# Optimization experiments

Hardware: AMD Instinct MI355X
Metric: run time of the kernel (lower is better)

## Reference

```python
import jax, jax.numpy as jnp
import numpy as np

N = 20000      # nodes (drugs, scaled to production size)
E = 640000     # edges
R = 65         # relation types
F_IN = 128     # input feature dim (trimnet embedding)
H1 = 64        # hidden1
H2 = 32        # hidden2 (bilinear discriminator dim)
B = 8192       # drug pairs in idx


def setup_inputs() -> dict:
    key = jax.random.key(0)
    ks = jax.random.split(key, 20)
    s = 0.05
    return {
        "x_o": jax.random.normal(ks[0], (N, F_IN), jnp.float32),
        "x_a": jax.random.normal(ks[1], (N, F_IN), jnp.float32),
        "features1": jax.random.normal(ks[2], (N, F_IN), jnp.float32),
        "W1": jax.random.normal(ks[3], (R, F_IN, H1), jnp.float32) * s,
        "root1": jax.random.normal(ks[4], (F_IN, H1), jnp.float32) * s,
        "b1": jnp.zeros((H1,), jnp.float32),
        "W2": jax.random.normal(ks[5], (R, H1, H2), jnp.float32) * s,
        "root2": jax.random.normal(ks[6], (H1, H2), jnp.float32) * s,
        "b2": jnp.zeros((H2,), jnp.float32),
        "attt": jnp.array([0.5, 0.5], jnp.float32),
        "disc_W": jax.random.normal(ks[7], (H2, H2), jnp.float32) * s,
        "disc_b": jnp.zeros((), jnp.float32),
        "cls_W": jax.random.normal(ks[8], (448, R), jnp.float32) * s,
        "cls_b": jnp.zeros((R,), jnp.float32),
        "edge_index": jax.random.randint(ks[9], (2, E), 0, N, jnp.int32),
        "e_type": jax.random.randint(ks[10], (E,), 0, R, jnp.int32),
        "e_type1": jax.random.randint(ks[11], (E,), 0, R, jnp.int32),
        "idx": jax.random.randint(ks[12], (2, B), 0, N, jnp.int32),
    }


def rgcn(x, src, dst, etype, W, root, b):
    """RGCNConv with per-relation mean aggregation (PyG default aggr='mean').
    Aggregates source features per (relation, dst) via one segment_sum, then
    applies the relation weights once with a batched matmul."""
    n, fin = x.shape
    seg = etype * n + dst                       # combined (relation, dst) segment id
    msg = x[src]                                # [E, fin] gather
    agg = jax.ops.segment_sum(msg, seg, num_segments=R * n).reshape(R, n, fin)
    cnt = jax.ops.segment_sum(jnp.ones((src.shape[0],), x.dtype), seg,
                              num_segments=R * n).reshape(R, n, 1)
    agg = agg / jnp.maximum(cnt, 1.0)           # per-relation mean
    out = jnp.einsum('rnf,rfh->nh', agg, W)     # sum over relations of W_r @ mean_r
    return out + x @ root + b


def reference(x_o, x_a, features1, W1, root1, b1, W2, root2, b2, attt,
              disc_W, disc_b, cls_W, cls_b, edge_index, e_type, e_type1, idx):
    src, dst = edge_index[0], edge_index[1]

    def enc(x, et):
        h1 = jax.nn.relu(rgcn(x, src, dst, et, W1, root1, b1))
        # dropout is identity in eval mode
        h2 = rgcn(h1, src, dst, et, W2, root2, b2)
        return h1, h2

    x1_o, x2_o = enc(x_o, e_type)
    _, x2_o_a = enc(x_a, e_type)
    _, x2_o_a_a = enc(x_o, e_type1)

    c = jax.nn.sigmoid(jnp.mean(x2_o, axis=0))  # readout + sigmoid, [H2]

    def disc(h_pl, h_mi):
        s1 = h_pl @ disc_W @ c + disc_b         # bilinear f_k(h, c)
        s2 = h_mi @ disc_W @ c + disc_b
        return jnp.stack([s1, s2], axis=1)      # [N, 2]

    ret_os = disc(x2_o, x2_o_a)
    ret_os_a = disc(x2_o, x2_o_a_a)

    final = jnp.concatenate([attt[0] * x1_o, attt[1] * x2_o], axis=1)  # [N, 96]
    e1 = jnp.concatenate([final[idx[0]], features1[idx[0]]], axis=1)   # [B, 224]
    e2 = jnp.concatenate([final[idx[1]], features1[idx[1]]], axis=1)
    log = jnp.concatenate([e1, e2], axis=1) @ cls_W + cls_b            # [B, 65]
    return (log, ret_os, ret_os_a, x2_o)
```

## Files before the change

kernel.cpp:

```cpp
#include <hip/hip_runtime.h>
#include <hip/hip_bf16.h>

#define NN 20000
#define EE 640000
#define RR 65
#define FIN1 128
#define HH1 64
#define HH2 32
#define BB 8192

constexpr int BM = 128;
constexpr int GBM = 256;
constexpr int NBH = 256;
constexpr int GRID_PRE = 2048;
constexpr int EPB = EE / NBH;
constexpr int NBT = (NN + BM - 1) / BM;
constexpr int NOCT = 8;
constexpr int NPO = NN / NOCT;
constexpr int NB2 = NOCT * RR;
constexpr int MAXT2 = EE / GBM + NB2;

constexpr int CLS_K  = 512;
constexpr int CLS_N  = 80;
constexpr int CLS_CK = 128;
constexpr int CLS_BM = 64;

typedef __attribute__((ext_vector_type(8))) short short8;
typedef __attribute__((ext_vector_type(4))) float floatx4;
typedef __attribute__((ext_vector_type(4))) unsigned int uint4e;
typedef __attribute__((ext_vector_type(2))) unsigned int uint2e;

constexpr size_t aln(size_t x) { return (x + 255) & ~(size_t)255; }

constexpr size_t OFF_CSUM  = 0;
constexpr size_t OFF_CNTD  = aln(OFF_CSUM + 32 * 4);
constexpr size_t ZERO_BYTES = OFF_CNTD + (size_t)NN * 4;
constexpr size_t OFF_DSTOFF = aln(ZERO_BYTES);
constexpr size_t OFF_BH0   = aln(OFF_DSTOFF + ((size_t)NN + 1) * 4);
constexpr size_t OFF_BH1   = OFF_BH0 + (size_t)NBH * NB2 * 4;
constexpr size_t OFF_BB0   = OFF_BH1 + (size_t)NBH * NB2 * 4;
constexpr size_t OFF_BB1   = OFF_BB0 + (size_t)NBH * NB2 * 4;
constexpr size_t OFF_HT    = aln(OFF_BB1 + (size_t)NBH * NB2 * 4);
constexpr size_t OFF_OFFB0 = aln(OFF_HT + (size_t)2 * NB2 * 4);
constexpr size_t OFF_OFFB1 = OFF_OFFB0 + (NB2 + 1) * 4;
constexpr size_t OFF_TILB0 = aln(OFF_OFFB1 + (NB2 + 1) * 4);
constexpr size_t OFF_TILT0 = OFF_TILB0 + (size_t)MAXT2 * 4;
constexpr size_t OFF_TILB1 = OFF_TILT0 + (size_t)MAXT2 * 4;
constexpr size_t OFF_TILT1 = OFF_TILB1 + (size_t)MAXT2 * 4;
// ... 21 lines not shown
constexpr size_t MSG_B2    = (size_t)EE * HH2 * 2;
constexpr size_t WS_END    = OFF_MSG + MSG_B1;

constexpr size_t O_LOG  = 0;
constexpr size_t O_ROS  = (size_t)BB * RR;
constexpr size_t O_ROSA = O_ROS + (size_t)NN * 2;
constexpr size_t O_X2O  = O_ROSA + (size_t)NN * 2;

__device__ inline unsigned short f2bf(float f) {
    __hip_bfloat16 h = __float2bfloat16(f);
    return *reinterpret_cast<unsigned short*>(&h);
}
__device__ inline float bfbits2f(unsigned int hi_bits) {
    return __uint_as_float(hi_bits);
}

struct GemmEnc {
    const unsigned short* X;
    unsigned short* msg;
    const unsigned int* perm;
    const int* offB;
    const int* tilB;
    const int* tilT;
};
struct GemmArgs { GemmEnc e[3]; };

struct RedEnc {
    const unsigned short* msg;
    const float* wD;
    float* base;
    unsigned short* bfout;
};
struct RedArgs { RedEnc e[3]; };

__global__ void k_hist(const int* __restrict__ ei, const int* __restrict__ et0,
                       const int* __restrict__ et1,
                       int* cntD, int* __restrict__ slotE,
                       int* __restrict__ bh0, int* __restrict__ bh1,
                       const float* __restrict__ x_o, const float* __restrict__ x_a,
                       const float* __restrict__ W1, const float* __restrict__ W2,
                       const float* __restrict__ root1, const float* __restrict__ root2,
                       const float* __restrict__ clsW,
                       unsigned short* xob, unsigned short* xab,
                       unsigned short* w1t, unsigned short* w2t,
                       unsigned short* r1t, unsigned short* r2t,
                       unsigned short* cwt) {
// ... 65 lines not shown
    for (int i4 = i0; i4 < NR2_4; i4 += stride) {
        int i = i4 * 4;
        int k = i % HH1; int hh = i / HH1;
        const float* s = &root2[(size_t)k * HH2 + hh];
        uint2 pk;
        pk.x = (unsigned)f2bf(s[0]) | ((unsigned)f2bf(s[HH2]) << 16);
        pk.y = (unsigned)f2bf(s[2 * HH2]) | ((unsigned)f2bf(s[3 * HH2]) << 16);
        ((uint2*)r2t)[i4] = pk;
    }
    const int NCW_4 = CLS_N * CLS_K / 4;
    for (int i4 = i0; i4 < NCW_4; i4 += stride) {
        int i = i4 * 4;
        int k = i % CLS_K; int n = i / CLS_K;
        uint2 pk = {0u, 0u};
        if (n < RR && k < 448) {
            const float* s = &clsW[(size_t)k * RR + n];
            pk.x = (unsigned)f2bf(s[0]) | ((unsigned)f2bf(s[RR]) << 16);
            pk.y = (unsigned)f2bf(s[2 * RR]) | ((unsigned)f2bf(s[3 * RR]) << 16);
        }
        ((uint2*)cwt)[i4] = pk;
    }
}

__global__ void k_scanD(const int* __restrict__ cntD, int* __restrict__ dstOff) {
    __shared__ int s[256];
    int t = threadIdx.x;
    constexpr int PER = (NN + 255) / 256;
    int lo = t * PER, hi = min(NN, lo + PER);
    int sum = 0;
    for (int i = lo; i < hi; i++) sum += cntD[i];
    s[t] = sum;
    __syncthreads();
    for (int ofs = 1; ofs < 256; ofs <<= 1) {
        int v = 0;
        if (t >= ofs) v = s[t - ofs];
        __syncthreads();
        if (t >= ofs) s[t] += v;
        __syncthreads();
    }
    int run = s[t] - sum;
    for (int i = lo; i < hi; i++) { dstOff[i] = run; run += cntD[i]; }
    if (t == 255) dstOff[NN] = run;
}

__global__ void k_post(const int* __restrict__ ei, const int* __restrict__ et0,
                       const int* __restrict__ et1, const int* __restrict__ dstOff,
                       const int* __restrict__ slotE,
                       int* __restrict__ posD, unsigned int* __restrict__ rdP) {
    int e = blockIdx.x * 256 + threadIdx.x;
    if (e < EE) {
        int d = ei[EE + e];
        int pos = dstOff[d] + slotE[e];
        posD[e] = pos;
        rdP[pos] = (unsigned)et0[e] | ((unsigned)et1[e] << 16);
    }
}

__global__ void k_scanB1(const int* __restrict__ bh0, const int* __restrict__ bh1,
                         int* __restrict__ bb0, int* __restrict__ bb1,
                         int* __restrict__ hT) {
    int w = (blockIdx.x * 256 + threadIdx.x) >> 6;
    int lane = threadIdx.x & 63;
    if (w >= 2 * NB2) return;
    int s = w / NB2, k = w % NB2;
    const int* bh = s ? bh1 : bh0;
    int* bb = s ? bb1 : bb0;
    int v[4];
    #pragma unroll
    for (int i = 0; i < 4; i++) v[i] = bh[(size_t)(lane * 4 + i) * NB2 + k];
    int ls = v[0] + v[1] + v[2] + v[3];
    int inc = ls;
    #pragma unroll
    for (int ofs = 1; ofs < 64; ofs <<= 1) {
        int o = __shfl_up(inc, ofs);
        if (lane >= ofs) inc += o;
    }
    int run = inc - ls;
    #pragma unroll
    for (int i = 0; i < 4; i++) {
        bb[(size_t)(lane * 4 + i) * NB2 + k] = run;
        run += v[i];
    }
    if (lane == 63) hT[s * NB2 + k] = run;
}

__global__ void k_scanB2(const int* __restrict__ hT,
                         int* offB0, int* offB1,
                         int* tilB0, int* tilT0, int* tilB1, int* tilT1) {
    __shared__ int h[2][NB2];
    __shared__ int o[2][NB2 + 1];
    __shared__ int to[2][NB2 + 1];
    __shared__ int csumE[2][8], csumT[2][8];
    int t = threadIdx.x;
    for (int p = t; p < 2 * NB2; p += 256) h[p / NB2][p % NB2] = hT[p];
    __syncthreads();
    if (t < 16) {
        int s = t / 8, c = t % 8;
        int runE = 0, runT = 0;
        for (int k = c * RR; k < (c + 1) * RR; k++) {
            o[s][k] = runE;  runE += h[s][k];
            to[s][k] = runT; runT += (h[s][k] + GBM - 1) / GBM;
        }
        csumE[s][c] = runE; csumT[s][c] = runT;
    }
    __syncthreads();
    if (t < 2) {
        int runE = 0, runT = 0;
        for (int c = 0; c < 8; c++) {
            int e = csumE[t][c], tt = csumT[t][c];
            csumE[t][c] = runE; csumT[t][c] = runT;
            runE += e; runT += tt;
        }
        o[t][NB2] = runE; to[t][NB2] = runT;
    }
    __syncthreads();
    if (t < 16) {
// ... 2 lines not shown
            o[s][k] += csumE[s][c];
            to[s][k] += csumT[s][c];
        }
    }
    __syncthreads();
    for (int p = t; p <= NB2; p += 256) { offB0[p] = o[0][p]; offB1[p] = o[1][p]; }
    for (int i = t; i < MAXT2; i += 256) {
        #pragma unroll
        for (int s = 0; s < 2; s++) {
            int total = to[s][NB2];
            int bkt = -1, ti = 0;
            if (i < total) {
                int lo = 0, hi = NB2;
                while (hi - lo > 1) { int mid = (lo + hi) >> 1; if (to[s][mid] <= i) lo = mid; else hi = mid; }
                bkt = lo;
                ti = i - to[s][lo];
            }
            if (s == 0) { tilB0[i] = bkt; tilT0[i] = ti; }
            else        { tilB1[i] = bkt; tilT1[i] = ti; }
        }
    }
}

__global__ void k_fillB(const int* __restrict__ ei, const int* __restrict__ et0,
                        const int* __restrict__ et1, const int* __restrict__ posD,
                        const int* __restrict__ offB0, const int* __restrict__ offB1,
                        const int* __restrict__ bb0, const int* __restrict__ bb1,
                        unsigned int* perm0, unsigned int* perm1) {
    __shared__ int lc[2][NB2];
    __shared__ int lb[2][NB2];
    int t = threadIdx.x;
    for (int p = t; p < NB2; p += 256) {
        lc[0][p] = 0; lc[1][p] = 0;
        lb[0][p] = offB0[p] + bb0[blockIdx.x * NB2 + p];
        lb[1][p] = offB1[p] + bb1[blockIdx.x * NB2 + p];
    }
    __syncthreads();
    int base = blockIdx.x * EPB;
    for (int i = t; i < EPB; i += 256) {
        int e = base + i;
        int src = ei[e];
        int pos = posD[e];
        int oct = src / NPO;
        unsigned int packed = ((unsigned)(src - oct * NPO) << 20) | (unsigned)pos;
        int k0 = oct * RR + et0[e];
        int k1 = oct * RR + et1[e];
        int p0 = atomicAdd(&lc[0][k0], 1);
        int p1 = atomicAdd(&lc[1][k1], 1);
        perm0[lb[0][k0] + p0] = packed;
        perm1[lb[1][k1] + p1] = packed;
    }
}

__global__ void k_wts(const int* __restrict__ dstOff, const unsigned int* __restrict__ rdP,
                      float* __restrict__ wD0, float* __restrict__ wD1) {
    constexpr int CAP = 96;
    __shared__ unsigned int ld[4][CAP];
    int wave = threadIdx.x >> 6;
    int lane = threadIdx.x & 63;
    int d = blockIdx.x * 4 + wave;
    int j0 = 0, deg = 0;
    if (d < NN) { j0 = dstOff[d]; deg = dstOff[d + 1] - j0; }
    for (int j = lane; j < deg && j < CAP; j += 64) ld[wave][j] = rdP[j0 + j];
    __syncthreads();
    for (int j = lane; j < deg; j += 64) {
        unsigned int my = (j < CAP) ? ld[wave][j] : rdP[j0 + j];
        unsigned int m0 = my & 0xffffu, m1 = my >> 16;
        int c0 = 0, c1 = 0;
        for (int k = 0; k < deg; k++) {
            unsigned int p = (k < CAP) ? ld[wave][k] : rdP[j0 + k];
            c0 += ((p & 0xffffu) == m0);
            c1 += ((p >> 16) == m1);
        }
        wD0[j0 + j] = 1.0f / (float)c0;
        wD1[j0 + j] = 1.0f / (float)c1;
    }
}

template <int FIN, int HOUT>
__launch_bounds__(256, 3)
__global__ void k_bgemm(const unsigned short* __restrict__ X0,
                        const unsigned short* __restrict__ X1,
                        const unsigned short* __restrict__ X2,
// ... 46 lines not shown
    for (int ks = 0; ks < KS; ks++) {
        int kk = ks * 32 + q * 8;
        short8 af0 = *(const short8*)&As[mbase + ln][kk];
        short8 af1 = *(const short8*)&As[mbase + 16 + ln][kk];
        #pragma unroll
        for (int nt = 0; nt < NT; nt++) {
            short8 bf = *(const short8*)&Bs[nt * 16 + ln][kk];
            acc[0][nt] = __builtin_amdgcn_mfma_f32_16x16x32_bf16(af0, bf, acc[0][nt], 0, 0, 0);
            acc[1][nt] = __builtin_amdgcn_mfma_f32_16x16x32_bf16(af1, bf, acc[1][nt], 0, 0, 0);
        }
    }

    #pragma unroll
    for (int mt = 0; mt < 2; mt++) {
        #pragma unroll
        for (int rr2 = 0; rr2 < 4; rr2++) {
            int i = mbase + mt * 16 + q * 4 + rr2;
            int n = n0 + i;
            if (i < mcount) {
                #pragma unroll
                for (int nt = 0; nt < NT; nt++)
                    O[(size_t)n * HOUT + nt * 16 + ln] = acc[mt][nt][rr2] + bias[nt * 16 + ln];
            }
        }
    }
}

template <int FIN, int HOUT>
__launch_bounds__(512, 8)
__global__ void k_gemm(GemmArgs ga, const unsigned short* __restrict__ WT) {
    const GemmEnc ge = ga.e[blockIdx.y];
    int b = blockIdx.x;
    int bkt = ge.tilB[b];
    if (bkt < 0) return;
    int r = bkt % RR;
    int srcBase = (bkt / RR) * NPO;
    int t = ge.tilT[b];
    int ebase = ge.offB[bkt] + t * GBM;
    int mcount = min(GBM, ge.offB[bkt + 1] - ebase);

    constexpr int LDK = FIN + 8;
    constexpr int LDM = HOUT + 8;
    constexpr int BSZ = HOUT * LDK;
    constexpr int MSZ = GBM * LDM;
    constexpr int USZ = BSZ > MSZ ? BSZ : MSZ;
    __shared__ unsigned short Us[USZ];
// ... 120 lines not shown
        re.base[o] = v0; re.base[o + 1] = v1; re.base[o + 2] = v2; re.base[o + 3] = v3;
        if (RELU) {
            re.bfout[o] = f2bf(v0); re.bfout[o + 1] = f2bf(v1);
            re.bfout[o + 2] = f2bf(v2); re.bfout[o + 3] = f2bf(v3);
        }
    }
}

__global__ void k_mean(const float* __restrict__ x2o, float* __restrict__ part) {
    __shared__ float s[256];
    int t = threadIdx.x; int hh = t & 31; int g = t >> 5;
    float acc = 0.f;
    for (int n = blockIdx.x * 8 + g; n < NN; n += gridDim.x * 8)
        acc += x2o[(size_t)n * 32 + hh];
    s[t] = acc;
    __syncthreads();
    if (t < 32) {
        float v = 0.f;
        for (int gg = 0; gg < 8; gg++) v += s[gg * 32 + t];
        part[blockIdx.x * 32 + t] = v;
    }
}

__global__ void k_csum(const float* __restrict__ part, float* __restrict__ csum) {
    int t = threadIdx.x;
    if (t < 32) {
        double a = 0.0;
        for (int b = 0; b < 256; b++) a += (double)part[b * 32 + t];
        csum[t] = (float)a;
    }
}

__global__ void k_disc(const float* __restrict__ x2o, const float* __restrict__ x2a,
                       const float* __restrict__ x2aa, const float* __restrict__ csum,
                       const float* __restrict__ discW, const float* __restrict__ discb,
                       float* ret_os, float* ret_osa) {
    __shared__ float c[32], v[32];
    int t = threadIdx.x;
    if (t < 32) c[t] = 1.f / (1.f + expf(-csum[t] * (1.f / NN)));
    __syncthreads();
    if (t < 32) {
        float a = 0.f;
        for (int j = 0; j < 32; j++) a += discW[t * 32 + j] * c[j];
        v[t] = a;
    }
    __syncthreads();
    float db = discb[0];
    int n = blockIdx.x * 256 + t;
    if (n < NN) {
        float s1 = 0.f, s2 = 0.f, s3 = 0.f;
        for (int j = 0; j < 32; j++) {
            float vj = v[j];
            s1 += x2o[(size_t)n * 32 + j] * vj;
            s2 += x2a[(size_t)n * 32 + j] * vj;
            s3 += x2aa[(size_t)n * 32 + j] * vj;
        }
        ret_os[n * 2] = s1 + db;  ret_os[n * 2 + 1] = s2 + db;
        ret_osa[n * 2] = s1 + db; ret_osa[n * 2 + 1] = s3 + db;
    }
}

__launch_bounds__(256, 2)
__global__ void k_clsg(const float* __restrict__ h1o, const float* __restrict__ x2o,
                       const float* __restrict__ feat, const float* __restrict__ attt,
                       const int* __restrict__ idx,
                       const unsigned short* __restrict__ cwt,
                       const float* __restrict__ clsb, float* __restrict__ log_out) {
    constexpr int LDK = CLS_CK + 8;
    __shared__ unsigned short As[CLS_BM][LDK];
    __shared__ unsigned short Bs[CLS_N][LDK];
    __shared__ int nd[2][CLS_BM];

    int tid = threadIdx.x;
    int p0 = blockIdx.x * CLS_BM;
    if (tid < CLS_BM) {
        nd[0][tid] = idx[p0 + tid];
        nd[1][tid] = idx[BB + p0 + tid];
    }
    float a0 = attt[0], a1 = attt[1];

    const int wave = tid >> 6;
    const int lane = tid & 63;
    const int q = lane >> 4;
    const int ln = lane & 15;
    constexpr int NT = CLS_N / 16;
    const int mbase = wave * 16;

    floatx4 acc[NT];
    #pragma unroll
    for (int nt = 0; nt < NT; nt++) acc[nt] = floatx4{0.f, 0.f, 0.f, 0.f};

    for (int ch = 0; ch < CLS_K / CLS_CK; ch++) {
        int kbase = ch * CLS_CK;
        __syncthreads();
        for (int c = tid; c < CLS_N * CLS_CK / 8; c += 256) {
            int row = c / (CLS_CK / 8), cc = c % (CLS_CK / 8);
            *(uint4*)&Bs[row][cc * 8] = *(const uint4*)&cwt[(size_t)row * CLS_K + kbase + cc * 8];
        }
        for (int c = tid; c < CLS_BM * CLS_CK / 4; c += 256) {
            int row = c / (CLS_CK / 4);
            int j4 = (c % (CLS_CK / 4)) * 4;
            int j = kbase + j4;
            float4 v = {0.f, 0.f, 0.f, 0.f};
            if (j < 448) {
                int hseg = j / 224, jj = j % 224;
                int node = nd[hseg][row];
                if (jj < 64) {
                    v = *(const float4*)&h1o[(size_t)node * 64 + jj];
                    v.x *= a0; v.y *= a0; v.z *= a0; v.w *= a0;
                } else if (jj < 96) {
                    v = *(const float4*)&x2o[(size_t)node * 32 + (jj - 64)];
                    v.x *= a1; v.y *= a1; v.z *= a1; v.w *= a1;
                } else {
                    v = *(const float4*)&feat[(size_t)node * 128 + (jj - 96)];
                }
            }
            uint2 pk;
            pk.x = (unsigned)f2bf(v.x) | ((unsigned)f2bf(v.y) << 16);
            pk.y = (unsigned)f2bf(v.z) | ((unsigned)f2bf(v.w) << 16);
            *(uint2*)&As[row][j4] = pk;
        }
        __syncthreads();
        #pragma unroll
        for (int ks = 0; ks < CLS_CK / 32; ks++) {
            int kk = ks * 32 + q * 8;
            short8 af = *(const short8*)&As[mbase + ln][kk];
            #pragma unroll
            for (int nt = 0; nt < NT; nt++) {
                short8 bf = *(const short8*)&Bs[nt * 16 + ln][kk];
                acc[nt] = __builtin_amdgcn_mfma_f32_16x16x32_bf16(af, bf, acc[nt], 0, 0, 0);
            }
        }
    }

    #pragma unroll
    for (int rr2 = 0; rr2 < 4; rr2++) {
        int i = mbase + q * 4 + rr2;
        int pair = p0 + i;
        #pragma unroll
        for (int nt = 0; nt < NT; nt++) {
            int col = nt * 16 + ln;
            if (col < RR)
                log_out[(size_t)pair * RR + col] = acc[nt][rr2] + clsb[col];
        }
    }
}

extern "C" void kernel_launch(void* const* d_in, const int* in_sizes, int n_in,
                              void* d_out, int out_size, void* d_ws, size_t ws_size,
                              hipStream_t stream) {
    const float* x_o   = (const float*)d_in[0];
    const float* x_a   = (const float*)d_in[1];
    const float* feat  = (const float*)d_in[2];
    const float* W1    = (const float*)d_in[3];
    const float* root1 = (const float*)d_in[4];
    const float* b1    = (const float*)d_in[5];
    const float* W2    = (const float*)d_in[6];
    const float* root2 = (const float*)d_in[7];
    const float* b2    = (const float*)d_in[8];
    const float* attt  = (const float*)d_in[9];
    const float* discW = (const float*)d_in[10];
    const float* discb = (const float*)d_in[11];
    const float* clsW  = (const float*)d_in[12];
    const float* clsb  = (const float*)d_in[13];
    const int* ei      = (const int*)d_in[14];
    const int* et0     = (const int*)d_in[15];
    const int* et1     = (const int*)d_in[16];
    const int* idx     = (const int*)d_in[17];

    char* ws = (char*)d_ws;
    float* csum = (float*)(ws + OFF_CSUM);
    int* cntD  = (int*)(ws + OFF_CNTD);
    int* dstOff = (int*)(ws + OFF_DSTOFF);
    int* bh0   = (int*)(ws + OFF_BH0);
    int* bh1   = (int*)(ws + OFF_BH1);
    int* bb0   = (int*)(ws + OFF_BB0);
    int* bb1   = (int*)(ws + OFF_BB1);
    int* hT    = (int*)(ws + OFF_HT);
    int* offB0 = (int*)(ws + OFF_OFFB0);
    int* offB1 = (int*)(ws + OFF_OFFB1);
    int* tilB0 = (int*)(ws + OFF_TILB0);
    int* tilT0 = (int*)(ws + OFF_TILT0);
    int* tilB1 = (int*)(ws + OFF_TILB1);
    int* tilT1 = (int*)(ws + OFF_TILT1);
    int* slotE = (int*)(ws + OFF_SLOT);
    int* posD  = (int*)(ws + OFF_POSD);
    unsigned int* rdP = (unsigned int*)(ws + OFF_RDP);
    float* wD0 = (float*)(ws + OFF_WD0);
    float* wD1 = (float*)(ws + OFF_WD1);
    unsigned int* perm0 = (unsigned int*)(ws + OFF_PERM0);
    unsigned int* perm1 = (unsigned int*)(ws + OFF_PERM1);
    unsigned short* xob = (unsigned short*)(ws + OFF_XOB);
    unsigned short* xab = (unsigned short*)(ws + OFF_XAB);
    float* h1o  = (float*)(ws + OFF_H1);
    float* h1a  = h1o + (size_t)NN * HH1;
    float* h1aa = h1a + (size_t)NN * HH1;
    unsigned short* h1bo  = (unsigned short*)(ws + OFF_H1B);
    unsigned short* h1ba  = h1bo + (size_t)NN * HH1;
    unsigned short* h1baa = h1ba + (size_t)NN * HH1;
    float* x2a  = (float*)(ws + OFF_X2A);
    float* x2aa = (float*)(ws + OFF_X2AA);
    unsigned short* w1t = (unsigned short*)(ws + OFF_W1BT);
    unsigned short* w2t = (unsigned short*)(ws + OFF_W2BT);
    unsigned short* r1t = (unsigned short*)(ws + OFF_R1T);
    unsigned short* r2t = (unsigned short*)(ws + OFF_R2T);
    unsigned short* cwt = (unsigned short*)(ws + OFF_CWT);
    float* part = (float*)(ws + OFF_PART);
    unsigned short* msg = (unsigned short*)(ws + OFF_MSG);

    float* out = (float*)d_out;
    float* log_out = out + O_LOG;
    float* ret_os  = out + O_ROS;
    float* ret_osa = out + O_ROSA;
    float* x2o     = out + O_X2O;

    size_t availMsg = ws_size > OFF_MSG ? ws_size - OFF_MSG : MSG_B1;
    int nb1 = (availMsg >= 2 * MSG_B1) ? 2 : 1;
    int nb2 = (availMsg >= 3 * MSG_B2) ? 3 : (availMsg >= 2 * MSG_B2 ? 2 : 1);

    hipMemsetAsync(ws, 0, ZERO_BYTES, stream);

    k_hist<<<GRID_PRE, 256, 0, stream>>>(ei, et0, et1, cntD, slotE, bh0, bh1,
                                         x_o, x_a, W1, W2, root1, root2, clsW,
                                         xob, xab, w1t, w2t, r1t, r2t, cwt);
    k_scanD<<<1, 256, 0, stream>>>(cntD, dstOff);
    k_post<<<2500, 256, 0, stream>>>(ei, et0, et1, dstOff, slotE, posD, rdP);
    k_scanB1<<<(2 * NB2 + 3) / 4, 256, 0, stream>>>(bh0, bh1, bb0, bb1, hT);
    k_scanB2<<<1, 256, 0, stream>>>(hT, offB0, offB1,
                                    tilB0, tilT0, tilB1, tilT1);
    k_fillB<<<NBH, 256, 0, stream>>>(ei, et0, et1, posD, offB0, offB1, bb0, bb1,
                                     perm0, perm1);
    k_wts<<<NN / 4, 256, 0, stream>>>(dstOff, rdP, wD0, wD1);

    {
        dim3 gb(NBT, 3);
        k_bgemm<FIN1, HH1><<<gb, 256, 0, stream>>>(xob, xab, xob, r1t, b1,
                                                   h1o, h1a, h1aa);
        const unsigned short* Xs[3] = {xob, xab, xob};
        float* Os[3] = {h1o, h1a, h1aa};
        unsigned short* Obs[3] = {h1bo, h1ba, h1baa};
        for (int e0 = 0; e0 < 3; ) {
            int g = 3 - e0 < nb1 ? 3 - e0 : nb1;
            GemmArgs ga{};
            RedArgs ra{};
            for (int j = 0; j < g; j++) {
                int enc = e0 + j;
                unsigned short* mb = msg + (size_t)j * EE * HH1;
                ga.e[j].X    = Xs[enc];
                ga.e[j].msg  = mb;
                ga.e[j].perm = enc == 2 ? perm1 : perm0;
                ga.e[j].offB = enc == 2 ? offB1 : offB0;
                ga.e[j].tilB = enc == 2 ? tilB1 : tilB0;
                ga.e[j].tilT = enc == 2 ? tilT1 : tilT0;
                ra.e[j].msg  = mb;
                ra.e[j].wD   = enc == 2 ? wD1 : wD0;
                ra.e[j].base = Os[enc];
                ra.e[j].bfout = Obs[enc];
            }
            k_gemm<FIN1, HH1><<<dim3(MAXT2, g), 512, 0, stream>>>(ga, w1t);
            k_reduce<HH1, true><<<dim3(NN / 4, g), 256, 0, stream>>>(ra, dstOff);
            e0 += g;
        }
    }

    {
        dim3 gb(NBT, 3);
        k_bgemm<HH1, HH2><<<gb, 256, 0, stream>>>(h1bo, h1ba, h1baa, r2t, b2,
                                                  x2o, x2a, x2aa);
        const unsigned short* Xs[3] = {h1bo, h1ba, h1baa};
        float* Os[3] = {x2o, x2a, x2aa};
        for (int e0 = 0; e0 < 3; ) {
            int g = 3 - e0 < nb2 ? 3 - e0 : nb2;
            GemmArgs ga{};
            RedArgs ra{};
            for (int j = 0; j < g; j++) {
                int enc = e0 + j;
                unsigned short* mb = msg + (size_t)j * EE * HH2;
                ga.e[j].X    = Xs[enc];
                ga.e[j].msg  = mb;
                ga.e[j].perm = enc == 2 ? perm1 : perm0;
                ga.e[j].offB = enc == 2 ? offB1 : offB0;
                ga.e[j].tilB = enc == 2 ? tilB1 : tilB0;
                ga.e[j].tilT = enc == 2 ? tilT1 : tilT0;
                ra.e[j].msg  = mb;
                ra.e[j].wD   = enc == 2 ? wD1 : wD0;
                ra.e[j].base = Os[enc];
                ra.e[j].bfout = nullptr;
            }
            k_gemm<HH1, HH2><<<dim3(MAXT2, g), 512, 0, stream>>>(ga, w2t);
            k_reduce<HH2, false><<<dim3(NN / 4, g), 256, 0, stream>>>(ra, dstOff);
            e0 += g;
        }
    }

    k_mean<<<256, 256, 0, stream>>>(x2o, part);
    k_csum<<<1, 64, 0, stream>>>(part, csum);
    k_disc<<<(NN + 255) / 256, 256, 0, stream>>>(x2o, x2a, x2aa, csum, discW, discb,
                                                 ret_os, ret_osa);
    k_clsg<<<BB / CLS_BM, 256, 0, stream>>>(h1o, x2o, feat, attt, idx, cwt, clsb, log_out);
}
```

Before: 555.8 us.

## Merge preprocessing, root-GEMM, and tail kernels into fewer block-partitioned launches

Independent kernels are merged into single launches that pick their role by block index: the dst scan with the bucket scan, the post pass with the tile-table build, the bucket fill with the degree-weight pass, and the classifier GEMM with the discriminator (which now folds in the readout sum). The root/bias GEMM is folded into the per-relation message GEMM launch, and layer 1 now processes all three encoders in one launch when workspace allows. The aim is to cut kernel launch count and the idle gaps between small dependent kernels. In exchange, each fused kernel carries the union of shared memory and register needs, which may lower occupancy, and layer 1 needs a larger message buffer.

```diff
diff --git a/kernel.cpp b/kernel.cpp
--- a/kernel.cpp
+++ b/kernel.cpp
@@ -24,6 +24,8 @@
 constexpr int CLS_N  = 80;
 constexpr int CLS_CK = 128;
 constexpr int CLS_BM = 64;
+constexpr int NCLSB  = BB / CLS_BM;
+constexpr int NDISCB = (NN + 255) / 256;
 
 typedef __attribute__((ext_vector_type(8))) short short8;
 typedef __attribute__((ext_vector_type(4))) float floatx4;
@@ -91,6 +93,7 @@
     const int* offB;
     const int* tilB;
     const int* tilT;
+    float* obase;
 };
 struct GemmArgs { GemmEnc e[3]; };
 
@@ -202,45 +205,33 @@
     }
 }
 
-__global__ void k_scanD(const int* __restrict__ cntD, int* __restrict__ dstOff) {
-    __shared__ int s[256];
+__global__ void k_scanA(const int* __restrict__ cntD, int* __restrict__ dstOff,
+                        const int* __restrict__ bh0, const int* __restrict__ bh1,
+                        int* __restrict__ bb0, int* __restrict__ bb1,
+                        int* __restrict__ hT) {
     int t = threadIdx.x;
-    constexpr int PER = (NN + 255) / 256;
-    int lo = t * PER, hi = min(NN, lo + PER);
-    int sum = 0;
-    for (int i = lo; i < hi; i++) sum += cntD[i];
-    s[t] = sum;
-    __syncthreads();
-    for (int ofs = 1; ofs < 256; ofs <<= 1) {
-        int v = 0;
-        if (t >= ofs) v = s[t - ofs];
+    if (blockIdx.x == 0) {
+        __shared__ int s[256];
+        constexpr int PER = (NN + 255) / 256;
+        int lo = t * PER, hi = min(NN, lo + PER);
+        int sum = 0;
+        for (int i = lo; i < hi; i++) sum += cntD[i];
+        s[t] = sum;
         __syncthreads();
-        if (t >= ofs) s[t] += v;
-        __syncthreads();
-    }
-    int run = s[t] - sum;
-    for (int i = lo; i < hi; i++) { dstOff[i] = run; run += cntD[i]; }
-    if (t == 255) dstOff[NN] = run;
-}
-
-__global__ void k_post(const int* __restrict__ ei, const int* __restrict__ et0,
-                       const int* __restrict__ et1, const int* __restrict__ dstOff,
-                       const int* __restrict__ slotE,
-                       int* __restrict__ posD, unsigned int* __restrict__ rdP) {
-    int e = blockIdx.x * 256 + threadIdx.x;
-    if (e < EE) {
-        int d = ei[EE + e];
-        int pos = dstOff[d] + slotE[e];
-        posD[e] = pos;
-        rdP[pos] = (unsigned)et0[e] | ((unsigned)et1[e] << 16);
-    }
-}
-
-__global__ void k_scanB1(const int* __restrict__ bh0, const int* __restrict__ bh1,
-                         int* __restrict__ bb0, int* __restrict__ bb1,
-                         int* __restrict__ hT) {
-    int w = (blockIdx.x * 256 + threadIdx.x) >> 6;
-    int lane = threadIdx.x & 63;
+        for (int ofs = 1; ofs < 256; ofs <<= 1) {
+            int v = 0;
+            if (t >= ofs) v = s[t - ofs];
+            __syncthreads();
+            if (t >= ofs) s[t] += v;
+            __syncthreads();
+        }
+        int run = s[t] - sum;
+        for (int i = lo; i < hi; i++) { dstOff[i] = run; run += cntD[i]; }
+        if (t == 255) dstOff[NN] = run;
+        return;
+    }
+    int w = (blockIdx.x - 1) * 4 + (t >> 6);
+    int lane = t & 63;
     if (w >= 2 * NB2) return;
     int s = w / NB2, k = w % NB2;
     const int* bh = s ? bh1 : bh0;
@@ -264,14 +255,28 @@
     if (lane == 63) hT[s * NB2 + k] = run;
 }
 
-__global__ void k_scanB2(const int* __restrict__ hT,
-                         int* offB0, int* offB1,
-                         int* tilB0, int* tilT0, int* tilB1, int* tilT1) {
+__global__ void k_postB(const int* __restrict__ ei, const int* __restrict__ et0,
+                        const int* __restrict__ et1, const int* __restrict__ dstOff,
+                        const int* __restrict__ slotE,
+                        int* __restrict__ posD, unsigned int* __restrict__ rdP,
+                        const int* __restrict__ hT,
+                        int* offB0, int* offB1,
+                        int* tilB0, int* tilT0, int* tilB1, int* tilT1) {
+    int t = threadIdx.x;
+    if (blockIdx.x < 2500) {
+        int e = blockIdx.x * 256 + t;
+        if (e < EE) {
+            int d = ei[EE + e];
+            int pos = dstOff[d] + slotE[e];
+            posD[e] = pos;
+            rdP[pos] = (unsigned)et0[e] | ((unsigned)et1[e] << 16);
+        }
+        return;
+    }
     __shared__ int h[2][NB2];
     __shared__ int o[2][NB2 + 1];
     __shared__ int to[2][NB2 + 1];
     __shared__ int csumE[2][8], csumT[2][8];
-    int t = threadIdx.x;
     for (int p = t; p < 2 * NB2; p += 256) h[p / NB2][p % NB2] = hT[p];
     __syncthreads();
     if (t < 16) {
@@ -320,43 +325,44 @@
     }
 }
 
-__global__ void k_fillB(const int* __restrict__ ei, const int* __restrict__ et0,
+__global__ void k_fillC(const int* __restrict__ ei, const int* __restrict__ et0,
                         const int* __restrict__ et1, const int* __restrict__ posD,
                         const int* __restrict__ offB0, const int* __restrict__ offB1,
                         const int* __restrict__ bb0, const int* __restrict__ bb1,
-                        unsigned int* perm0, unsigned int* perm1) {
-    __shared__ int lc[2][NB2];
-    __shared__ int lb[2][NB2];
+                        unsigned int* perm0, unsigned int* perm1,
+                        const int* __restrict__ dstOff, const unsigned int* __restrict__ rdP,
+                        float* __restrict__ wD0, float* __restrict__ wD1) {
     int t = threadIdx.x;
-    for (int p = t; p < NB2; p += 256) {
-        lc[0][p] = 0; lc[1][p] = 0;
-        lb[0][p] = offB0[p] + bb0[blockIdx.x * NB2 + p];
-        lb[1][p] = offB1[p] + bb1[blockIdx.x * NB2 + p];
-    }
-    __syncthreads();
-    int base = blockIdx.x * EPB;
-    for (int i = t; i < EPB; i += 256) {
-        int e = base + i;
-        int src = ei[e];
-        int pos = posD[e];
-        int oct = src / NPO;
-        unsigned int packed = ((unsigned)(src - oct * NPO) << 20) | (unsigned)pos;
-        int k0 = oct * RR + et0[e];
-        int k1 = oct * RR + et1[e];
-        int p0 = atomicAdd(&lc[0][k0], 1);
-        int p1 = atomicAdd(&lc[1][k1], 1);
-        perm0[lb[0][k0] + p0] = packed;
-        perm1[lb[1][k1] + p1] = packed;
-    }
-}
-
-__global__ void k_wts(const int* __restrict__ dstOff, const unsigned int* __restrict__ rdP,
-                      float* __restrict__ wD0, float* __restrict__ wD1) {
+    if (blockIdx.x < NBH) {
+        __shared__ int lc[2][NB2];
+        __shared__ int lb[2][NB2];
+        for (int p = t; p < NB2; p += 256) {
+            lc[0][p] = 0; lc[1][p] = 0;
+            lb[0][p] = offB0[p] + bb0[blockIdx.x * NB2 + p];
+            lb[1][p] = offB1[p] + bb1[blockIdx.x * NB2 + p];
+        }
+        __syncthreads();
+        int base = blockIdx.x * EPB;
+        for (int i = t; i < EPB; i += 256) {
+            int e = base + i;
+            int src = ei[e];
+            int pos = posD[e];
+            int oct = src / NPO;
+            unsigned int packed = ((unsigned)(src - oct * NPO) << 20) | (unsigned)pos;
+            int k0 = oct * RR + et0[e];
+            int k1 = oct * RR + et1[e];
+            int p0 = atomicAdd(&lc[0][k0], 1);
+            int p1 = atomicAdd(&lc[1][k1], 1);
+            perm0[lb[0][k0] + p0] = packed;
+            perm1[lb[1][k1] + p1] = packed;
+        }
+        return;
+    }
     constexpr int CAP = 96;
     __shared__ unsigned int ld[4][CAP];
-    int wave = threadIdx.x >> 6;
-    int lane = threadIdx.x & 63;
-    int d = blockIdx.x * 4 + wave;
+    int wave = t >> 6;
+    int lane = t & 63;
+    int d = (blockIdx.x - NBH) * 4 + wave;
     int j0 = 0, deg = 0;
     if (d < NN) { j0 = dstOff[d]; deg = dstOff[d + 1] - j0; }
     for (int j = lane; j < deg && j < CAP; j += 64) ld[wave][j] = rdP[j0 + j];
@@ -449,6 +455,160 @@
                 for (int nt = 0; nt < NT; nt++)
                     O[(size_t)n * HOUT + nt * 16 + ln] = acc[mt][nt][rr2] + bias[nt * 16 + ln];
             }
+        }
+    }
+}
+
+template <int FIN, int HOUT>
+__launch_bounds__(512, 8)
+__global__ void k_mgemm(GemmArgs ga, const unsigned short* __restrict__ WT,
+                        const unsigned short* __restrict__ rootT,
+                        const float* __restrict__ bias) {
+    const GemmEnc ge = ga.e[blockIdx.y];
+    constexpr int LDK = FIN + 8;
+    constexpr int LDM = HOUT + 8;
+    constexpr int BSZ = HOUT * LDK;
+    constexpr int MSZ = GBM * LDM;
+    constexpr int USZ = BSZ > MSZ ? BSZ : MSZ;
+    __shared__ unsigned short Us[USZ];
+    __shared__ int Sr[GBM];
+    __shared__ int Pd[GBM];
+
+    int tid = threadIdx.x;
+    const int wave = tid >> 6;
+    const int lane = tid & 63;
+    const int q = lane >> 4;
+    const int ln = lane & 15;
+    constexpr int NT = HOUT / 16;
+    constexpr int KS = FIN / 32;
+
+    if (blockIdx.x < NBT) {
+        int n0 = blockIdx.x * BM;
+        int mcount = min(BM, NN - n0);
+        {
+            constexpr int CHB = HOUT * FIN / 8;
+            for (int c = tid; c < CHB; c += 512) {
+                int row = c / (FIN / 8), cc = c % (FIN / 8);
+                *(uint4*)&Us[row * LDK + cc * 8] = *(const uint4*)&rootT[row * FIN + cc * 8];
+            }
+        }
+        __syncthreads();
+        const int mbase = wave * 16;
+        int i = mbase + ln;
+        short8 A[KS];
+        #pragma unroll
+        for (int ks = 0; ks < KS; ks++) A[ks] = short8{0,0,0,0,0,0,0,0};
+        if (i < mcount) {
+            const unsigned short* ap = ge.X + (size_t)(n0 + i) * FIN + q * 8;
+            #pragma unroll
+            for (int ks = 0; ks < KS; ks++) A[ks] = *(const short8*)(ap + ks * 32);
+        }
+        floatx4 acc[NT];
+        #pragma unroll
+        for (int nt = 0; nt < NT; nt++) acc[nt] = floatx4{0.f, 0.f, 0.f, 0.f};
+        #pragma unroll
+        for (int ks = 0; ks < KS; ks++) {
+            int kk = ks * 32 + q * 8;
+            #pragma unroll
+            for (int nt = 0; nt < NT; nt++) {
+                short8 bf = *(const short8*)&Us[(nt * 16 + ln) * LDK + kk];
+                acc[nt] = __builtin_amdgcn_mfma_f32_16x16x32_bf16(A[ks], bf, acc[nt], 0, 0, 0);
+            }
+        }
+        #pragma unroll
+        for (int rr2 = 0; rr2 < 4; rr2++) {
+            int i2 = mbase + q * 4 + rr2;
+            if (i2 < mcount) {
+                #pragma unroll
+                for (int nt = 0; nt < NT; nt++)
+                    ge.obase[(size_t)(n0 + i2) * HOUT + nt * 16 + ln] = acc[nt][rr2] + bias[nt * 16 + ln];
+            }
+        }
+        return;
+    }
+
+    int b = blockIdx.x - NBT;
+    int bkt = ge.tilB[b];
+    if (bkt < 0) return;
+    int r = bkt % RR;
+    int srcBase = (bkt / RR) * NPO;
+    int t = ge.tilT[b];
+    int ebase = ge.offB[bkt] + t * GBM;
+    int mcount = min(GBM, ge.offB[bkt + 1] - ebase);
+
+    if (tid < GBM) {
+        if (tid < mcount) {
+            unsigned int p = ge.perm[ebase + tid];
+            Sr[tid] = srcBase + (int)(p >> 20);
+            Pd[tid] = (int)(p & 0xFFFFFu);
+        } else { Sr[tid] = -1; Pd[tid] = 0; }
+    }
+    {
+        const unsigned short* Wr = WT + (size_t)r * HOUT * FIN;
+        constexpr int CHB = HOUT * FIN / 8;
+        for (int c = tid; c < CHB; c += 512) {
+            int row = c / (FIN / 8), cc = c % (FIN / 8);
+            *(uint4*)&Us[row * LDK + cc * 8] = *(const uint4*)&Wr[row * FIN + cc * 8];
+        }
+    }
+    __syncthreads();
+
+    const int mbase = wave * 32;
+
+    int s0 = Sr[mbase + ln];
+    int s1 = Sr[mbase + 16 + ln];
+    short8 A0[KS], A1[KS];
+    #pragma unroll
+    for (int ks = 0; ks < KS; ks++) {
+        A0[ks] = short8{0,0,0,0,0,0,0,0};
+        A1[ks] = short8{0,0,0,0,0,0,0,0};
+    }
+    if (s0 >= 0) {
+        const unsigned short* ap = ge.X + (size_t)s0 * FIN + q * 8;
+        #pragma unroll
+        for (int ks = 0; ks < KS; ks++) A0[ks] = *(const short8*)(ap + ks * 32);
+    }
+    if (s1 >= 0) {
+        const unsigned short* ap = ge.X + (size_t)s1 * FIN + q * 8;
+        #pragma unroll
+        for (int ks = 0; ks < KS; ks++) A1[ks] = *(const short8*)(ap + ks * 32);
+    }
+
+    floatx4 acc[2][NT];
+    #pragma unroll
+    for (int a = 0; a < 2; a++)
+        #pragma unroll
+        for (int nt = 0; nt < NT; nt++) acc[a][nt] = floatx4{0.f, 0.f, 0.f, 0.f};
+
+    #pragma unroll
+    for (int ks = 0; ks < KS; ks++) {
+        int kk = ks * 32 + q * 8;
+        #pragma unroll
+        for (int nt = 0; nt < NT; nt++) {
+            short8 bf = *(const short8*)&Us[(nt * 16 + ln) * LDK + kk];
+            acc[0][nt] = __builtin_amdgcn_mfma_f32_16x16x32_bf16(A0[ks], bf, acc[0][nt], 0, 0, 0);
+            acc[1][nt] = __builtin_amdgcn_mfma_f32_16x16x32_bf16(A1[ks], bf, acc[1][nt], 0, 0, 0);
+        }
+    }
+
+    __syncthreads();
+    #pragma unroll
+    for (int mt = 0; mt < 2; mt++) {
+        #pragma unroll
+        for (int rr2 = 0; rr2 < 4; rr2++) {
+            int i = mbase + mt * 16 + q * 4 + rr2;
+            #pragma unroll
+            for (int nt = 0; nt < NT; nt++)
+                Us[i * LDM + nt * 16 + ln] = f2bf(acc[mt][rr2 >= 0 ? nt : nt][rr2]);
+        }
+    }
+    __syncthreads();
+    constexpr int CH = HOUT / 8;
+    for (int c = tid; c < GBM * CH; c += 512) {
+        int row = c / CH, cc = c % CH;
+        if (row < mcount) {
+            uint4e v = *(const uint4e*)&Us[row * LDM + cc * 8];
+            *(uint4e*)&ge.msg[(size_t)Pd[row] * HOUT + cc * 8] = v;
         }
     }
 }
@@ -615,31 +775,121 @@
     }
 }
 
-__global__ void k_csum(const float* __restrict__ part, float* __restrict__ csum) {
-    int t = threadIdx.x;
-    if (t < 32) {
+__launch_bounds__(256, 2)
+__global__ void k_dc(const float* __restrict__ h1o, const float* __restrict__ x2o,
+                     const float* __restrict__ feat, const float* __restrict__ attt,
+                     const int* __restrict__ idx,
+                     const unsigned short* __restrict__ cwt,
+                     const float* __restrict__ clsb, float* __restrict__ log_out,
+                     const float* __restrict__ part,
+                     const float* __restrict__ x2a, const float* __restrict__ x2aa,
+                     const float* __restrict__ discW, const float* __restrict__ discb,
+                     float* ret_os, float* ret_osa) {
+    int tid = threadIdx.x;
+    if (blockIdx.x < NCLSB) {
+        constexpr int LDK = CLS_CK + 8;
+        __shared__ unsigned short As[CLS_BM][LDK];
+        __shared__ unsigned short Bs[CLS_N][LDK];
+        __shared__ int nd[2][CLS_BM];
+
+        int p0 = blockIdx.x * CLS_BM;
+        if (tid < CLS_BM) {
+            nd[0][tid] = idx[p0 + tid];
+            nd[1][tid] = idx[BB + p0 + tid];
+        }
+        float a0 = attt[0], a1 = attt[1];
+
+        const int wave = tid >> 6;
+        const int lane = tid & 63;
+        const int q = lane >> 4;
+        const int ln = lane & 15;
+        constexpr int NT = CLS_N / 16;
+        const int mbase = wave * 16;
+
+        floatx4 acc[NT];
+        #pragma unroll
+        for (int nt = 0; nt < NT; nt++) acc[nt] = floatx4{0.f, 0.f, 0.f, 0.f};
+
+        for (int ch = 0; ch < CLS_K / CLS_CK; ch++) {
+            int kbase = ch * CLS_CK;
+            __syncthreads();
+            for (int c = tid; c < CLS_N * CLS_CK / 8; c += 256) {
+                int row = c / (CLS_CK / 8), cc = c % (CLS_CK / 8);
+                *(uint4*)&Bs[row][cc * 8] = *(const uint4*)&cwt[(size_t)row * CLS_K + kbase + cc * 8];
+            }
+            for (int c = tid; c < CLS_BM * CLS_CK / 4; c += 256) {
+                int row = c / (CLS_CK / 4);
+                int j4 = (c % (CLS_CK / 4)) * 4;
+                int j = kbase + j4;
+                float4 v = {0.f, 0.f, 0.f, 0.f};
+                if (j < 448) {
+                    int hseg = j / 224, jj = j % 224;
+                    int node = nd[hseg][row];
+                    if (jj < 64) {
+                        v = *(const float4*)&h1o[(size_t)node * 64 + jj];
+                        v.x *= a0; v.y *= a0; v.z *= a0; v.w *= a0;
+                    } else if (jj < 96) {
+                        v = *(const float4*)&x2o[(size_t)node * 32 + (jj - 64)];
+                        v.x *= a1; v.y *= a1; v.z *= a1; v.w *= a1;
+                    } else {
+                        v = *(const float4*)&feat[(size_t)node * 128 + (jj - 96)];
+                    }
+                }
+                uint2 pk;
+                pk.x = (unsigned)f2bf(v.x) | ((unsigned)f2bf(v.y) << 16);
+                pk.y = (unsigned)f2bf(v.z) | ((unsigned)f2bf(v.w) << 16);
+                *(uint2*)&As[row][j4] = pk;
+            }
+            __syncthreads();
+            #pragma unroll
+            for (int ks = 0; ks < CLS_CK / 32; ks++) {
+                int kk = ks * 32 + q * 8;
+                short8 af = *(const short8*)&As[mbase + ln][kk];
+                #pragma unroll
+                for (int nt = 0; nt < NT; nt++) {
+                    short8 bf = *(const short8*)&Bs[nt * 16 + ln][kk];
+                    acc[nt] = __builtin_amdgcn_mfma_f32_16x16x32_bf16(af, bf, acc[nt], 0, 0, 0);
+                }
+            }
+        }
+
+        #pragma unroll
+        for (int rr2 = 0; rr2 < 4; rr2++) {
+            int i = mbase + q * 4 + rr2;
+            int pair = p0 + i;
+            #pragma unroll
+            for (int nt = 0; nt < NT; nt++) {
+                int col = nt * 16 + ln;
+                if (col < RR)
+                    log_out[(size_t)pair * RR + col] = acc[nt][rr2] + clsb[col];
+            }
+        }
+        return;
+    }
+
+    __shared__ double sd[256];
+    __shared__ float c[32], v[32];
+    {
+        int g = tid >> 5, hh = tid & 31;
         double a = 0.0;
-        for (int b = 0; b < 256; b++) a += (double)part[b * 32 + t];
-        csum[t] = (float)a;
-    }
-}
-
-__global__ void k_disc(const float* __restrict__ x2o, const float* __restrict__ x2a,
-                       const float* __restrict__ x2aa, const float* __restrict__ csum,
-                       const float* __restrict__ discW, const float* __restrict__ discb,
-                       float* ret_os, float* ret_osa) {
-    __shared__ float c[32], v[32];
-    int t = threadIdx.x;
-    if (t < 32) c[t] = 1.f / (1.f + expf(-csum[t] * (1.f / NN)));
-    __syncthreads();
-    if (t < 32) {
-        float a = 0.f;
-        for (int j = 0; j < 32; j++) a += discW[t * 32 + j] * c[j];
-        v[t] = a;
-    }
-    __syncthreads();
+        for (int k = 0; k < 32; k++) a += (double)part[(size_t)(k * 8 + g) * 32 + hh];
+        sd[tid] = a;
+        __syncthreads();
+        if (tid < 32) {
+            double a2 = 0.0;
+            for (int gg = 0; gg < 8; gg++) a2 += sd[gg * 32 + tid];
+            c[tid] = 1.f / (1.f + expf(-(float)a2 * (1.f / NN)));
+        }
+        __syncthreads();
+        if (tid < 32) {
+            float a3 = 0.f;
+            for (int j = 0; j < 32; j++) a3 += discW[tid * 32 + j] * c[j];
+            v[tid] = a3;
+        }
+        __syncthreads();
+    }
     float db = discb[0];
-    int n = blockIdx.x * 256 + t;
+    int n = (blockIdx.x - NCLSB) * 256 + tid;
     if (n < NN) {
         float s1 = 0.f, s2 = 0.f, s3 = 0.f;
         for (int j = 0; j < 32; j++) {
@@ -650,92 +900,6 @@
         }
         ret_os[n * 2] = s1 + db;  ret_os[n * 2 + 1] = s2 + db;
         ret_osa[n * 2] = s1 + db; ret_osa[n * 2 + 1] = s3 + db;
-    }
-}
-
-__launch_bounds__(256, 2)
-__global__ void k_clsg(const float* __restrict__ h1o, const float* __restrict__ x2o,
-                       const float* __restrict__ feat, const float* __restrict__ attt,
-                       const int* __restrict__ idx,
-                       const unsigned short* __restrict__ cwt,
-                       const float* __restrict__ clsb, float* __restrict__ log_out) {
-    constexpr int LDK = CLS_CK + 8;
-    __shared__ unsigned short As[CLS_BM][LDK];
-    __shared__ unsigned short Bs[CLS_N][LDK];
-    __shared__ int nd[2][CLS_BM];
-
-    int tid = threadIdx.x;
-    int p0 = blockIdx.x * CLS_BM;
-    if (tid < CLS_BM) {
-        nd[0][tid] = idx[p0 + tid];
-        nd[1][tid] = idx[BB + p0 + tid];
-    }
-    float a0 = attt[0], a1 = attt[1];
-
-    const int wave = tid >> 6;
-    const int lane = tid & 63;
-    const int q = lane >> 4;
-    const int ln = lane & 15;
-    constexpr int NT = CLS_N / 16;
-    const int mbase = wave * 16;
-
-    floatx4 acc[NT];
-    #pragma unroll
-    for (int nt = 0; nt < NT; nt++) acc[nt] = floatx4{0.f, 0.f, 0.f, 0.f};
-
-    for (int ch = 0; ch < CLS_K / CLS_CK; ch++) {
-        int kbase = ch * CLS_CK;
-        __syncthreads();
-        for (int c = tid; c < CLS_N * CLS_CK / 8; c += 256) {
-            int row = c / (CLS_CK / 8), cc = c % (CLS_CK / 8);
-            *(uint4*)&Bs[row][cc * 8] = *(const uint4*)&cwt[(size_t)row * CLS_K + kbase + cc * 8];
-        }
-        for (int c = tid; c < CLS_BM * CLS_CK / 4; c += 256) {
-            int row = c / (CLS_CK / 4);
-            int j4 = (c % (CLS_CK / 4)) * 4;
-            int j = kbase + j4;
-            float4 v = {0.f, 0.f, 0.f, 0.f};
-            if (j < 448) {
-                int hseg = j / 224, jj = j % 224;
-                int node = nd[hseg][row];
-                if (jj < 64) {
-                    v = *(const float4*)&h1o[(size_t)node * 64 + jj];
-                    v.x *= a0; v.y *= a0; v.z *= a0; v.w *= a0;
-                } else if (jj < 96) {
-                    v = *(const float4*)&x2o[(size_t)node * 32 + (jj - 64)];
-                    v.x *= a1; v.y *= a1; v.z *= a1; v.w *= a1;
-                } else {
-                    v = *(const float4*)&feat[(size_t)node * 128 + (jj - 96)];
-                }
-            }
-            uint2 pk;
-            pk.x = (unsigned)f2bf(v.x) | ((unsigned)f2bf(v.y) << 16);
-            pk.y = (unsigned)f2bf(v.z) | ((unsigned)f2bf(v.w) << 16);
-            *(uint2*)&As[row][j4] = pk;
-        }
-        __syncthreads();
-        #pragma unroll
-        for (int ks = 0; ks < CLS_CK / 32; ks++) {
-            int kk = ks * 32 + q * 8;
-            short8 af = *(const short8*)&As[mbase + ln][kk];
-            #pragma unroll
-            for (int nt = 0; nt < NT; nt++) {
-                short8 bf = *(const short8*)&Bs[nt * 16 + ln][kk];
-                acc[nt] = __builtin_amdgcn_mfma_f32_16x16x32_bf16(af, bf, acc[nt], 0, 0, 0);
-            }
-        }
-    }
-
-    #pragma unroll
-    for (int rr2 = 0; rr2 < 4; rr2++) {
-        int i = mbase + q * 4 + rr2;
-        int pair = p0 + i;
-        #pragma unroll
-        for (int nt = 0; nt < NT; nt++) {
-            int col = nt * 16 + ln;
-            if (col < RR)
-                log_out[(size_t)pair * RR + col] = acc[nt][rr2] + clsb[col];
-        }
     }
 }
 
@@ -762,7 +926,6 @@
     const int* idx     = (const int*)d_in[17];
 
     char* ws = (char*)d_ws;
-    float* csum = (float*)(ws + OFF_CSUM);
     int* cntD  = (int*)(ws + OFF_CNTD);
     int* dstOff = (int*)(ws + OFF_DSTOFF);
     int* bh0   = (int*)(ws + OFF_BH0);
@@ -808,7 +971,7 @@
     float* x2o     = out + O_X2O;
 
     size_t availMsg = ws_size > OFF_MSG ? ws_size - OFF_MSG : MSG_B1;
-    int nb1 = (availMsg >= 2 * MSG_B1) ? 2 : 1;
+    int nb1 = (availMsg >= 3 * MSG_B1) ? 3 : (availMsg >= 2 * MSG_B1 ? 2 : 1);
     int nb2 = (availMsg >= 3 * MSG_B2) ? 3 : (availMsg >= 2 * MSG_B2 ? 2 : 1);
 
     hipMemsetAsync(ws, 0, ZERO_BYTES, stream);
@@ -816,22 +979,36 @@
     k_hist<<<GRID_PRE, 256, 0, stream>>>(ei, et0, et1, cntD, slotE, bh0, bh1,
                                          x_o, x_a, W1, W2, root1, root2, clsW,
                                          xob, xab, w1t, w2t, r1t, r2t, cwt);
-    k_scanD<<<1, 256, 0, stream>>>(cntD, dstOff);
-    k_post<<<2500, 256, 0, stream>>>(ei, et0, et1, dstOff, slotE, posD, rdP);
-    k_scanB1<<<(2 * NB2 + 3) / 4, 256, 0, stream>>>(bh0, bh1, bb0, bb1, hT);
-    k_scanB2<<<1, 256, 0, stream>>>(hT, offB0, offB1,
-                                    tilB0, tilT0, tilB1, tilT1);
-    k_fillB<<<NBH, 256, 0, stream>>>(ei, et0, et1, posD, offB0, offB1, bb0, bb1,
-                                     perm0, perm1);
-    k_wts<<<NN / 4, 256, 0, stream>>>(dstOff, rdP, wD0, wD1);
-
-    {
+    k_scanA<<<1 + (2 * NB2 + 3) / 4, 256, 0, stream>>>(cntD, dstOff, bh0, bh1,
+                                                       bb0, bb1, hT);
+    k_postB<<<2501, 256, 0, stream>>>(ei, et0, et1, dstOff, slotE, posD, rdP,
+                                      hT, offB0, offB1, tilB0, tilT0, tilB1, tilT1);
+    k_fillC<<<NBH + NN / 4, 256, 0, stream>>>(ei, et0, et1, posD, offB0, offB1,
+                                              bb0, bb1, perm0, perm1,
+                                              dstOff, rdP, wD0, wD1);
+
+    const unsigned short* X1s[3] = {xob, xab, xob};
+    float* O1s[3] = {h1o, h1a, h1aa};
+    unsigned short* O1bs[3] = {h1bo, h1ba, h1baa};
+    const unsigned short* X2s[3] = {h1bo, h1ba, h1baa};
+    float* O2s[3] = {x2o, x2a, x2aa};
+
+    if (nb1 >= 3) {
+        GemmArgs ga{};
+        RedArgs ra{};
+        for (int enc = 0; enc < 3; enc++) {
+            unsigned short* mb = msg + (size_t)enc * EE * HH1;
+            ga.e[enc] = GemmEnc{X1s[enc], mb, enc == 2 ? perm1 : perm0,
+                                enc == 2 ? offB1 : offB0, enc == 2 ? tilB1 : tilB0,
+                                enc == 2 ? tilT1 : tilT0, O1s[enc]};
+            ra.e[enc] = RedEnc{mb, enc == 2 ? wD1 : wD0, O1s[enc], O1bs[enc]};
+        }
+        k_mgemm<FIN1, HH1><<<dim3(NBT + MAXT2, 3), 512, 0, stream>>>(ga, w1t, r1t, b1);
+        k_reduce<HH1, true><<<dim3(NN / 4, 3), 256, 0, stream>>>(ra, dstOff);
+    } else {
         dim3 gb(NBT, 3);
         k_bgemm<FIN1, HH1><<<gb, 256, 0, stream>>>(xob, xab, xob, r1t, b1,
                                                    h1o, h1a, h1aa);
-        const unsigned short* Xs[3] = {xob, xab, xob};
-        float* Os[3] = {h1o, h1a, h1aa};
-        unsigned short* Obs[3] = {h1bo, h1ba, h1baa};
         for (int e0 = 0; e0 < 3; ) {
             int g = 3 - e0 < nb1 ? 3 - e0 : nb1;
             GemmArgs ga{};
@@ -839,16 +1016,10 @@
             for (int j = 0; j < g; j++) {
                 int enc = e0 + j;
                 unsigned short* mb = msg + (size_t)j * EE * HH1;
-                ga.e[j].X    = Xs[enc];
-                ga.e[j].msg  = mb;
-                ga.e[j].perm = enc == 2 ? perm1 : perm0;
-                ga.e[j].offB = enc == 2 ? offB1 : offB0;
-                ga.e[j].tilB = enc == 2 ? tilB1 : tilB0;
-                ga.e[j].tilT = enc == 2 ? tilT1 : tilT0;
-                ra.e[j].msg  = mb;
-                ra.e[j].wD   = enc == 2 ? wD1 : wD0;
-                ra.e[j].base = Os[enc];
-                ra.e[j].bfout = Obs[enc];
+                ga.e[j] = GemmEnc{X1s[enc], mb, enc == 2 ? perm1 : perm0,
+                                  enc == 2 ? offB1 : offB0, enc == 2 ? tilB1 : tilB0,
+                                  enc == 2 ? tilT1 : tilT0, O1s[enc]};
+                ra.e[j] = RedEnc{mb, enc == 2 ? wD1 : wD0, O1s[enc], O1bs[enc]};
             }
             k_gemm<FIN1, HH1><<<dim3(MAXT2, g), 512, 0, stream>>>(ga, w1t);
             k_reduce<HH1, true><<<dim3(NN / 4, g), 256, 0, stream>>>(ra, dstOff);
@@ -856,12 +1027,22 @@
         }
     }
 
-    {
+    if (nb2 >= 3) {
+        GemmArgs ga{};
+        RedArgs ra{};
+        for (int enc = 0; enc < 3; enc++) {
+            unsigned short* mb = msg + (size_t)enc * EE * HH2;
+            ga.e[enc] = GemmEnc{X2s[enc], mb, enc == 2 ? perm1 : perm0,
+                                enc == 2 ? offB1 : offB0, enc == 2 ? tilB1 : tilB0,
+                                enc == 2 ? tilT1 : tilT0, O2s[enc]};
+            ra.e[enc] = RedEnc{mb, enc == 2 ? wD1 : wD0, O2s[enc], nullptr};
+        }
+        k_mgemm<HH1, HH2><<<dim3(NBT + MAXT2, 3), 512, 0, stream>>>(ga, w2t, r2t, b2);
+        k_reduce<HH2, false><<<dim3(NN / 4, 3), 256, 0, stream>>>(ra, dstOff);
+    } else {
         dim3 gb(NBT, 3);
         k_bgemm<HH1, HH2><<<gb, 256, 0, stream>>>(h1bo, h1ba, h1baa, r2t, b2,
                                                   x2o, x2a, x2aa);
-        const unsigned short* Xs[3] = {h1bo, h1ba, h1baa};
-        float* Os[3] = {x2o, x2a, x2aa};
         for (int e0 = 0; e0 < 3; ) {
             int g = 3 - e0 < nb2 ? 3 - e0 : nb2;
             GemmArgs ga{};
@@ -869,16 +1050,10 @@
             for (int j = 0; j < g; j++) {
                 int enc = e0 + j;
                 unsigned short* mb = msg + (size_t)j * EE * HH2;
-                ga.e[j].X    = Xs[enc];
-                ga.e[j].msg  = mb;
-                ga.e[j].perm = enc == 2 ? perm1 : perm0;
-                ga.e[j].offB = enc == 2 ? offB1 : offB0;
-                ga.e[j].tilB = enc == 2 ? tilB1 : tilB0;
-                ga.e[j].tilT = enc == 2 ? tilT1 : tilT0;
-                ra.e[j].msg  = mb;
-                ra.e[j].wD   = enc == 2 ? wD1 : wD0;
-                ra.e[j].base = Os[enc];
-                ra.e[j].bfout = nullptr;
+                ga.e[j] = GemmEnc{X2s[enc], mb, enc == 2 ? perm1 : perm0,
+                                  enc == 2 ? offB1 : offB0, enc == 2 ? tilB1 : tilB0,
+                                  enc == 2 ? tilT1 : tilT0, O2s[enc]};
+                ra.e[j] = RedEnc{mb, enc == 2 ? wD1 : wD0, O2s[enc], nullptr};
             }
             k_gemm<HH1, HH2><<<dim3(MAXT2, g), 512, 0, stream>>>(ga, w2t);
             k_reduce<HH2, false><<<dim3(NN / 4, g), 256, 0, stream>>>(ra, dstOff);
@@ -887,8 +1062,7 @@
     }
 
     k_mean<<<256, 256, 0, stream>>>(x2o, part);
-    k_csum<<<1, 64, 0, stream>>>(part, csum);
-    k_disc<<<(NN + 255) / 256, 256, 0, stream>>>(x2o, x2a, x2aa, csum, discW, discb,
-                                                 ret_os, ret_osa);
-    k_clsg<<<BB / CLS_BM, 256, 0, stream>>>(h1o, x2o, feat, attt, idx, cwt, clsb, log_out);
-}
+    k_dc<<<NCLSB + NDISCB, 256, 0, stream>>>(h1o, x2o, feat, attt, idx, cwt, clsb,
+                                             log_out, part, x2a, x2aa, discW, discb,
+                                             ret_os, ret_osa);
+}
```

New measurement: 522.5 us. 6.0% less time.
